# Kernel tuning notes

Hardware: AMD Instinct MI355X
Metric: run time of the kernel (lower is better)

Reference implementation:

```python
import jax, jax.numpy as jnp
import numpy as np

NUM_CLASSES = 80
BATCH_PER_IMG = 512          # cfg.MODEL.ROI_HEADS.BATCH_SIZE_PER_IMAGE
POS_FRAC = 0.25              # cfg.MODEL.ROI_HEADS.POSITIVE_FRACTION
NUM_FG_TARGET = int(BATCH_PER_IMG * POS_FRAC)  # 128
IOU_THRESH = 0.5             # cfg.MODEL.ROI_HEADS.IOU_THRESHOLDS = [0.5], labels [0,1]

B, M, N = 64, 100, 4000      # images, gt boxes/img, proposals/img
K = N + M                    # proposal_append_gt=True


def _make_boxes(key, shape, lo=0.0, hi=800.0, wh_max=256.0):
    k1, k2 = jax.random.split(key)
    xy = jax.random.uniform(k1, shape, minval=lo, maxval=hi)
    wh = jax.random.uniform(k2, shape, minval=8.0, maxval=wh_max)
    return jnp.concatenate([xy, xy + wh], axis=-1)  # [..., 4] = x1,y1,x2,y2


def setup_inputs() -> dict:
    key = jax.random.key(0)
    kg, kp, kc, kr = jax.random.split(key, 4)
    gt_boxes = _make_boxes(kg, (B, M, 2))
    proposal_boxes = _make_boxes(kp, (B, N, 2))
    gt_classes = jax.random.randint(kc, (B, M), 0, NUM_CLASSES, dtype=jnp.int32).astype(jnp.int64)
    rand_priority = jax.random.uniform(kr, (B, K), dtype=jnp.float32)
    return {
        'gt_boxes': gt_boxes,
        'proposal_boxes': proposal_boxes,
        'gt_classes': gt_classes,
        'rand_priority': rand_priority,
    }


def pairwise_iou(a, b):
    # a: [M,4], b: [K,4] -> [M,K]
    area_a = (a[:, 2] - a[:, 0]) * (a[:, 3] - a[:, 1])          # [M]
    area_b = (b[:, 2] - b[:, 0]) * (b[:, 3] - b[:, 1])          # [K]
    lt = jnp.maximum(a[:, None, :2], b[None, :, :2])            # [M,K,2]
    rb = jnp.minimum(a[:, None, 2:], b[None, :, 2:])            # [M,K,2]
    wh = jnp.clip(rb - lt, 0.0)
    inter = wh[..., 0] * wh[..., 1]                              # [M,K]
    union = area_a[:, None] + area_b[None, :] - inter
    return jnp.where(inter > 0, inter / union, 0.0)


def _per_image(gt_b, prop_b, gt_cls, pri):
    # proposal_append_gt: concat gt boxes onto proposals
    boxes = jnp.concatenate([prop_b, gt_b], axis=0)              # [K,4]
    quality = pairwise_iou(gt_b, boxes)                          # [M,K]
    matched_vals = quality.max(axis=0)                           # [K]
    matched_idxs = quality.argmax(axis=0)                        # [K]
    matched_labels = matched_vals >= IOU_THRESH                  # label 1 = fg, 0 = bg
    # gt_classes[matched_idxs]; bg gets label num_classes
    cls = jnp.where(matched_labels, gt_cls[matched_idxs], NUM_CLASSES)  # [K]
    fg = matched_labels
    bg = ~matched_labels
    num_fg = jnp.minimum(NUM_FG_TARGET, fg.sum())
    num_bg = jnp.minimum(BATCH_PER_IMG - num_fg, bg.sum())
    # randperm-equivalent: sort a shared random priority, masked per group
    fg_order = jnp.argsort(jnp.where(fg, pri, -1.0))[::-1]       # fg indices first
    bg_order = jnp.argsort(jnp.where(bg, pri, -1.0))[::-1]
    pos = jnp.arange(BATCH_PER_IMG)
    idx = jnp.where(pos < num_fg, fg_order[pos],
                    bg_order[jnp.clip(pos - num_fg, 0, K - 1)])
    valid = pos < (num_fg + num_bg)
    s_iou = jnp.where(valid, matched_vals[idx], 0.0)
    s_idx = jnp.where(valid, idx, -1)
    s_cls = jnp.where(valid, cls[idx], -1)
    s_gt = jnp.where(valid, matched_idxs[idx], -1)
    return s_iou, s_idx, s_cls, s_gt, valid


def reference(gt_boxes, proposal_boxes, gt_classes, rand_priority):
    return jax.vmap(_per_image)(gt_boxes, proposal_boxes,
                                gt_classes.astype(jnp.int32), rand_priority)
```

## Files before the change

### kernel.cpp

```cpp
#include <hip/hip_runtime.h>
#include <stdint.h>

#define B_IMG        64
#define M_GT         100
#define N_PROP       4000
#define K_TOT        4100
#define NUM_CLASSES_ 80
#define BATCH_PER    512
#define NUM_FG_TGT   128
#define OUT_STRIDE   (B_IMG * BATCH_PER)

#define NT1          256
#define BPI1         33
#define EPB1         128
#define NTH          1024
#define HALF_CAP     1024
#define KITER        ((K_TOT + NTH - 1) / NTH)
#define NTF          1024


__device__ __forceinline__ float iou_a(float4 g, float area_a,
                                       float bx1, float by1, float bx2, float by2,
                                       float area_b) {
#pragma clang fp contract(off)
    float ltx = fmaxf(g.x, bx1), lty = fmaxf(g.y, by1);
    float rbx = fminf(g.z, bx2), rby = fminf(g.w, by2);
    float wx = fmaxf(rbx - ltx, 0.0f);
    float wy = fmaxf(rby - lty, 0.0f);
    float inter = wx * wy;
    float uni = area_a + area_b - inter;
    return inter / uni;
}

__device__ __forceinline__ float iou_g(float4 g,
                                       float bx1, float by1, float bx2, float by2,
                                       float area_b) {
#pragma clang fp contract(off)
    float area_a = (g.z - g.x) * (g.w - g.y);
    float ltx = fmaxf(g.x, bx1), lty = fmaxf(g.y, by1);
    float rbx = fminf(g.z, bx2), rby = fminf(g.w, by2);
    float wx = fmaxf(rbx - ltx, 0.0f);
    float wy = fmaxf(rby - lty, 0.0f);
    float inter = wx * wy;
    float uni = area_a + area_b - inter;
    return inter / uni;
}

__device__ __forceinline__ float box_area(float4 g) {
#pragma clang fp contract(off)
    return (g.z - g.x) * (g.w - g.y);
}

__global__ __launch_bounds__(NT1, 8) void match_kernel(
        const float* __restrict__ gt_boxes,
        const float* __restrict__ prop_boxes,
        const float* __restrict__ rand_pri,
        uint64_t*    __restrict__ keys)
{
    __shared__ float4 s_gtb4[M_GT];
    __shared__ float  s_gta[M_GT];

    const int blk = blockIdx.x;
    const int b   = blk / BPI1;
    const int q   = blk % BPI1;
    const int tid = threadIdx.x;

    for (int i = tid; i < M_GT; i += NT1)
        s_gtb4[i] = ((const float4*)gt_boxes)[(size_t)b * M_GT + i];
    __syncthreads();
    for (int i = tid; i < M_GT; i += NT1)
        s_gta[i] = box_area(s_gtb4[i]);
    __syncthreads();

    const int e    = q * EPB1 + (tid >> 1);
    const int half = tid & 1;
    if (e >= K_TOT) return;

    const uint32_t pb = __float_as_uint(rand_pri[(size_t)b * K_TOT + e]);
    float4 bp;
    if (e < N_PROP)
        bp = *(const float4*)(prop_boxes + ((size_t)b * N_PROP + e) * 4);
    else
        bp = s_gtb4[e - N_PROP];
    const float area_b = box_area(bp);
    const int mlo = half * (M_GT / 2);
    float best = -1.0f; int bidx = mlo;
#pragma unroll 2
    for (int m = mlo; m < mlo + M_GT / 2; ++m) {
        float iv = iou_a(s_gtb4[m], s_gta[m], bp.x, bp.y, bp.z, bp.w, area_b);
        if (iv > best) { best = iv; bidx = m; }
    }
    const float ob = __shfl_xor(best, 1);
    const int   oi = __shfl_xor(bidx, 1);
    if (half == 0) {
        if (ob > best) { best = ob; bidx = oi; }
        const bool fg = best >= 0.5f;
        uint64_t key = (fg ? (1ull << 50) : 0ull)
                     | ((uint64_t)pb << 20)
                     | ((uint64_t)e  << 7)
                     | (uint64_t)bidx;
        __hip_atomic_store(&keys[(size_t)b * K_TOT + e], key,
                           __ATOMIC_RELAXED, __HIP_MEMORY_SCOPE_AGENT);
    }
}

__global__ __launch_bounds__(NTH) void select_kernel(
        const float* __restrict__ gt_boxes,
        const float* __restrict__ prop_boxes,
        const int*   __restrict__ gt_classes,
        const uint64_t* __restrict__ keys,
        float*       __restrict__ out)
{
    __shared__ uint64_t s_keys[K_TOT];
    __shared__ uint64_t s_cand[2 * HALF_CAP];
    __shared__ int      s_hist[2][256];
    __shared__ float4   s_gtb4[M_GT];
    __shared__ float    s_gta[M_GT];
    __shared__ int      s_gtc[M_GT];
    __shared__ float    s_out[5][BATCH_PER];
    __shared__ int      s_T[2], s_needed[2], s_cnt[2];

    const int b   = blockIdx.x;
    const int tid = threadIdx.x;

    __builtin_amdgcn_fence(__ATOMIC_ACQUIRE, "agent");

    for (int i = tid; i < 512; i += NTH) s_hist[i >> 8][i & 255] = 0;
    if (tid < 2) s_cnt[tid] = 0;
    for (int i = tid; i < M_GT; i += NTH) {
        s_gtb4[i] = ((const float4*)gt_boxes)[(size_t)b * M_GT + i];
        s_gtc[i]  = gt_classes[(size_t)b * M_GT + i];
    }
    __syncthreads();
    for (int i = tid; i < M_GT; i += NTH)
        s_gta[i] = box_area(s_gtb4[i]);

#pragma unroll
    for (int kb = 0; kb < KITER; ++kb) {
        int k = kb * NTH + tid;
        if (k < K_TOT) {
            uint64_t key = keys[(size_t)b * K_TOT + k];
            s_keys[k] = key;
            int g = ((key >> 50) & 1ull) ? 0 : 1;
            uint32_t pbits = (uint32_t)((key >> 20) & 0x3FFFFFFFull);
            int bucket = min(255, (int)(__uint_as_float(pbits) * 256.0f));
            atomicAdd(&s_hist[g][bucket], 1);
        }
    }
    __syncthreads();

    for (int d = 1; d < 256; d <<= 1) {
        int v = 0, g = tid >> 8, t = tid & 255;
        bool act = (tid < 512) && (t + d < 256);
        if (act) v = s_hist[g][t + d];
        __syncthreads();
        if (act) s_hist[g][t] += v;
        __syncthreads();
    }

    if (tid == 0) {
        int fg_total = s_hist[0][0];
        int bg_total = s_hist[1][0];
        int nfg = min(NUM_FG_TGT, fg_total);
        int nbg = min(BATCH_PER - nfg, bg_total);
        s_needed[0] = nfg; s_needed[1] = nbg;
    }
    __syncthreads();

    if (tid < 512) {
        int g = tid >> 8, t = tid & 255;
        int need = s_needed[g];
        int St  = s_hist[g][t];
        int St1 = (t == 255) ? -1 : s_hist[g][t + 1];
        if (St >= need && St1 < need) s_T[g] = t;
    }
    if (tid < BATCH_PER) {
        s_out[0][tid] = 0.0f; s_out[1][tid] = -1.0f;
        s_out[2][tid] = -1.0f; s_out[3][tid] = -1.0f;
    }
    __syncthreads();

    const int nfg = s_needed[0], nbg = s_needed[1];
    if (tid < BATCH_PER)
        s_out[4][tid] = (tid < nfg + nbg) ? 1.0f : 0.0f;

    const int lane = tid & 63;
    const uint64_t ltm = (1ull << lane) - 1ull;
#pragma unroll
    for (int kb = 0; kb < KITER; ++kb) {
        int k = kb * NTH + tid;
        bool in = k < K_TOT;
        uint64_t key = in ? s_keys[k] : 0ull;
        bool isfg = in && (((key >> 50) & 1ull) != 0ull);
        bool sel = false;
        if (in) {
            uint32_t pbits = (uint32_t)((key >> 20) & 0x3FFFFFFFull);
            int bucket = min(255, (int)(__uint_as_float(pbits) * 256.0f));
            sel = bucket >= s_T[isfg ? 0 : 1];
        }
        const bool sf = sel && isfg;
        const bool sb = sel && !isfg;
        const uint64_t bf = __ballot(sf);
        const uint64_t bb = __ballot(sb);
        int basef = 0, baseb = 0;
        if (lane == 0) {
            if (bf) basef = atomicAdd(&s_cnt[0], (int)__popcll(bf));
            if (bb) baseb = atomicAdd(&s_cnt[1], (int)__popcll(bb));
        }
        basef = __shfl(basef, 0);
        baseb = __shfl(baseb, 0);
        if (sf) {
            int pos = basef + (int)__popcll(bf & ltm);
            if (pos < HALF_CAP) s_cand[pos] = key;
        }
        if (sb) {
            int pos = baseb + (int)__popcll(bb & ltm);
            if (pos < HALF_CAP) s_cand[HALF_CAP + pos] = key;
        }
    }
    __syncthreads();

    const int fgc = min(s_cnt[0], HALF_CAP);
    const int bgc = min(s_cnt[1], HALF_CAP);
    for (int c = tid; c < fgc + bgc; c += NTH) {
        const bool isfg = (c < fgc);
        const int  base = isfg ? 0 : HALF_CAP;
        const int  cnt  = isfg ? fgc : bgc;
        const int  ci   = isfg ? c : (c - fgc);
        const uint64_t kc = s_cand[base + ci];
        int r = 0;
        for (int j = 0; j < cnt; ++j)
            r += (s_cand[base + j] > kc) ? 1 : 0;
        int slot = -1;
        if (isfg) { if (r < nfg) slot = r; }
        else      { if (r < nbg) slot = nfg + r; }
        if (slot >= 0) {
            int idx = (int)((kc >> 7) & 0x1FFFull);
            int mi  = (int)(kc & 0x7Full);
            float4 bp;
            if (idx < N_PROP)
                bp = *(const float4*)(prop_boxes + ((size_t)b * N_PROP + idx) * 4);
            else
                bp = s_gtb4[idx - N_PROP];
            const float area_b = box_area(bp);
            float iou = iou_a(s_gtb4[mi], s_gta[mi], bp.x, bp.y, bp.z, bp.w, area_b);
            s_out[0][slot] = iou;
            s_out[1][slot] = (float)idx;
            s_out[2][slot] = (float)(isfg ? s_gtc[mi] : NUM_CLASSES_);
            s_out[3][slot] = (float)mi;
        }
    }
    __syncthreads();

    for (int i = tid; i < 5 * BATCH_PER; i += NTH) {
        int o = i / BATCH_PER, p = i % BATCH_PER;
        out[(size_t)o * OUT_STRIDE + (size_t)b * BATCH_PER + p] = s_out[o][p];
    }
}

__global__ __launch_bounds__(NTF) void roiheads_fallback(
        const float* __restrict__ gt_boxes,
        const float* __restrict__ prop_boxes,
        const int*   __restrict__ gt_classes,
        const float* __restrict__ rand_pri,
        float*       __restrict__ out)
{
    __shared__ uint64_t s_keys[K_TOT];
    __shared__ uint64_t s_cand[2 * HALF_CAP];
    __shared__ int      s_hist[2][256];
    __shared__ float4   s_gtb4[M_GT];
    __shared__ int      s_gtc[M_GT];
    __shared__ float    s_out[5][BATCH_PER];
    __shared__ int      s_T[2], s_needed[2], s_cnt[2];

    const int b   = blockIdx.x;
    const int tid = threadIdx.x;

    for (int i = tid; i < 512; i += NTF) s_hist[i >> 8][i & 255] = 0;
    if (tid < 2) s_cnt[tid] = 0;
    for (int i = tid; i < M_GT; i += NTF) {
        s_gtb4[i] = ((const float4*)gt_boxes)[(size_t)b * M_GT + i];
        s_gtc[i]  = gt_classes[(size_t)b * M_GT + i];
    }
    __syncthreads();

    for (int k = tid; k < K_TOT; k += NTF) {
        float4 bp;
        if (k < N_PROP)
            bp = *(const float4*)(prop_boxes + ((size_t)b * N_PROP + k) * 4);
        else
            bp = s_gtb4[k - N_PROP];
        const float area_b = box_area(bp);
        float best = -1.0f; int bidx = 0;
        for (int m = 0; m < M_GT; ++m) {
            float iv = iou_g(s_gtb4[m], bp.x, bp.y, bp.z, bp.w, area_b);
            if (iv > best) { best = iv; bidx = m; }
        }
        const bool fg = best >= 0.5f;
        const float pri = rand_pri[(size_t)b * K_TOT + k];
        const uint32_t pb = __float_as_uint(pri);
        s_keys[k] = (fg ? (1ull << 50) : 0ull)
                  | ((uint64_t)pb << 20)
                  | ((uint64_t)k  << 7)
                  | (uint64_t)bidx;
        int bucket = min(255, (int)(pri * 256.0f));
        atomicAdd(&s_hist[fg ? 0 : 1][bucket], 1);
    }
    __syncthreads();

    for (int d = 1; d < 256; d <<= 1) {
        int v = 0, g = tid >> 8, t = tid & 255;
        bool act = (tid < 512) && (t + d < 256);
        if (act) v = s_hist[g][t + d];
        __syncthreads();
        if (act) s_hist[g][t] += v;
        __syncthreads();
    }

    if (tid == 0) {
        int fg_total = s_hist[0][0];
        int bg_total = s_hist[1][0];
        int nfg = min(NUM_FG_TGT, fg_total);
        int nbg = min(BATCH_PER - nfg, bg_total);
        s_needed[0] = nfg; s_needed[1] = nbg;
    }
    __syncthreads();

    if (tid < 512) {
        int g = tid >> 8, t = tid & 255;
        int need = s_needed[g];
        int St  = s_hist[g][t];
        int St1 = (t == 255) ? -1 : s_hist[g][t + 1];
        if (St >= need && St1 < need) s_T[g] = t;
    }
    if (tid < BATCH_PER) {
        s_out[0][tid] = 0.0f; s_out[1][tid] = -1.0f;
        s_out[2][tid] = -1.0f; s_out[3][tid] = -1.0f;
    }
    __syncthreads();

    const int nfg = s_needed[0], nbg = s_needed[1];
    if (tid < BATCH_PER)
        s_out[4][tid] = (tid < nfg + nbg) ? 1.0f : 0.0f;

    for (int k = tid; k < K_TOT; k += NTF) {
        uint64_t key = s_keys[k];
        int g = ((key >> 50) & 1ull) ? 0 : 1;
        uint32_t pbits = (uint32_t)((key >> 20) & 0x3FFFFFFFull);
        int bucket = min(255, (int)(__uint_as_float(pbits) * 256.0f));
        if (bucket >= s_T[g]) {
            int pos = atomicAdd(&s_cnt[g], 1);
            if (pos < HALF_CAP) s_cand[g * HALF_CAP + pos] = key;
        }
    }
    __syncthreads();

    const int fgc = min(s_cnt[0], HALF_CAP);
    const int bgc = min(s_cnt[1], HALF_CAP);
    for (int c = tid; c < fgc + bgc; c += NTF) {
        const bool isfg = (c < fgc);
        const int  base = isfg ? 0 : HALF_CAP;
        const int  cnt  = isfg ? fgc : bgc;
        const int  ci   = isfg ? c : (c - fgc);
        const uint64_t kc = s_cand[base + ci];
        int r = 0;
        for (int j = 0; j < cnt; ++j)
            r += (s_cand[base + j] > kc) ? 1 : 0;
        int slot = -1;
        if (isfg) { if (r < nfg) slot = r; }
        else      { if (r < nbg) slot = nfg + r; }
        if (slot >= 0) {
            int idx = (int)((kc >> 7) & 0x1FFFull);
            int mi  = (int)(kc & 0x7Full);
            float4 bp;
            if (idx < N_PROP)
                bp = *(const float4*)(prop_boxes + ((size_t)b * N_PROP + idx) * 4);
            else
                bp = s_gtb4[idx - N_PROP];
            const float area_b = box_area(bp);
            float iou = iou_g(s_gtb4[mi], bp.x, bp.y, bp.z, bp.w, area_b);
            s_out[0][slot] = iou;
            s_out[1][slot] = (float)idx;
            s_out[2][slot] = (float)(isfg ? s_gtc[mi] : NUM_CLASSES_);
            s_out[3][slot] = (float)mi;
        }
    }
    __syncthreads();

    for (int i = tid; i < 5 * BATCH_PER; i += NTF) {
        int o = i / BATCH_PER, p = i % BATCH_PER;
        out[(size_t)o * OUT_STRIDE + (size_t)b * BATCH_PER + p] = s_out[o][p];
    }
}

extern "C" void kernel_launch(void* const* d_in, const int* in_sizes, int n_in,
                              void* d_out, int out_size, void* d_ws, size_t ws_size,
                              hipStream_t stream) {
    const float* gt_boxes   = (const float*)d_in[0];
    const float* prop_boxes = (const float*)d_in[1];
    const int*   gt_classes = (const int*)  d_in[2];
    const float* rand_pri   = (const float*)d_in[3];
    float* out = (float*)d_out;

    const size_t need_ws = (size_t)B_IMG * K_TOT * sizeof(uint64_t);
    if (d_ws != nullptr && ws_size >= need_ws) {
        uint64_t* keys = (uint64_t*)d_ws;
        match_kernel<<<B_IMG * BPI1, NT1, 0, stream>>>(gt_boxes, prop_boxes,
                                                       rand_pri, keys);
        select_kernel<<<B_IMG, NTH, 0, stream>>>(gt_boxes, prop_boxes,
                                                 gt_classes, keys, out);
    } else {
        roiheads_fallback<<<B_IMG, NTF, 0, stream>>>(gt_boxes, prop_boxes,
                                                     gt_classes, rand_pri, out);
    }
}
```

Baseline: 105.2 us.

## Use one thread per proposal in matching and simplify candidate compaction

The matching kernel now gives each proposal a single thread that loops over all 100 GT boxes, reading them from global memory rather than shared memory, instead of splitting the GT range across two lanes and merging with shuffles. The grid per image drops from 33 to 17 blocks. The select kernel's ballot/popcount wave-aggregated compaction is replaced by plain per-thread shared atomics. This removes the shuffle and merge overhead and some synchronisation, but halves thread-level parallelism in matching and adds contention on the shared atomics.

```diff
diff --git a/kernel.cpp b/kernel.cpp
--- a/kernel.cpp
+++ b/kernel.cpp
@@ -11,8 +11,7 @@
 #define OUT_STRIDE   (B_IMG * BATCH_PER)
 
 #define NT1          256
-#define BPI1         33
-#define EPB1         128
+#define BPI1         17
 #define NTH          1024
 #define HALF_CAP     1024
 #define KITER        ((K_TOT + NTH - 1) / NTH)
@@ -57,23 +56,20 @@
         const float* __restrict__ rand_pri,
         uint64_t*    __restrict__ keys)
 {
-    __shared__ float4 s_gtb4[M_GT];
-    __shared__ float  s_gta[M_GT];
+    __shared__ float s_gta[M_GT];
 
     const int blk = blockIdx.x;
     const int b   = blk / BPI1;
     const int q   = blk % BPI1;
     const int tid = threadIdx.x;
 
+    const float4* gtb = (const float4*)gt_boxes + (size_t)b * M_GT;
+
     for (int i = tid; i < M_GT; i += NT1)
-        s_gtb4[i] = ((const float4*)gt_boxes)[(size_t)b * M_GT + i];
-    __syncthreads();
-    for (int i = tid; i < M_GT; i += NT1)
-        s_gta[i] = box_area(s_gtb4[i]);
-    __syncthreads();
-
-    const int e    = q * EPB1 + (tid >> 1);
-    const int half = tid & 1;
+        s_gta[i] = box_area(gtb[i]);
+    __syncthreads();
+
+    const int e = q * NT1 + tid;
     if (e >= K_TOT) return;
 
     const uint32_t pb = __float_as_uint(rand_pri[(size_t)b * K_TOT + e]);
@@ -81,27 +77,23 @@
     if (e < N_PROP)
         bp = *(const float4*)(prop_boxes + ((size_t)b * N_PROP + e) * 4);
     else
-        bp = s_gtb4[e - N_PROP];
+        bp = gtb[e - N_PROP];
     const float area_b = box_area(bp);
-    const int mlo = half * (M_GT / 2);
-    float best = -1.0f; int bidx = mlo;
-#pragma unroll 2
-    for (int m = mlo; m < mlo + M_GT / 2; ++m) {
-        float iv = iou_a(s_gtb4[m], s_gta[m], bp.x, bp.y, bp.z, bp.w, area_b);
+
+    float best = -1.0f; int bidx = 0;
+#pragma unroll 4
+    for (int m = 0; m < M_GT; ++m) {
+        const float4 g = gtb[m];
+        float iv = iou_a(g, s_gta[m], bp.x, bp.y, bp.z, bp.w, area_b);
         if (iv > best) { best = iv; bidx = m; }
     }
-    const float ob = __shfl_xor(best, 1);
-    const int   oi = __shfl_xor(bidx, 1);
-    if (half == 0) {
-        if (ob > best) { best = ob; bidx = oi; }
-        const bool fg = best >= 0.5f;
-        uint64_t key = (fg ? (1ull << 50) : 0ull)
-                     | ((uint64_t)pb << 20)
-                     | ((uint64_t)e  << 7)
-                     | (uint64_t)bidx;
-        __hip_atomic_store(&keys[(size_t)b * K_TOT + e], key,
-                           __ATOMIC_RELAXED, __HIP_MEMORY_SCOPE_AGENT);
-    }
+    const bool fg = best >= 0.5f;
+    uint64_t key = (fg ? (1ull << 50) : 0ull)
+                 | ((uint64_t)pb << 20)
+                 | ((uint64_t)e  << 7)
+                 | (uint64_t)bidx;
+    __hip_atomic_store(&keys[(size_t)b * K_TOT + e], key,
+                       __ATOMIC_RELAXED, __HIP_MEMORY_SCOPE_AGENT);
 }
 
 __global__ __launch_bounds__(NTH) void select_kernel(
@@ -184,38 +176,14 @@
     if (tid < BATCH_PER)
         s_out[4][tid] = (tid < nfg + nbg) ? 1.0f : 0.0f;
 
-    const int lane = tid & 63;
-    const uint64_t ltm = (1ull << lane) - 1ull;
-#pragma unroll
-    for (int kb = 0; kb < KITER; ++kb) {
-        int k = kb * NTH + tid;
-        bool in = k < K_TOT;
-        uint64_t key = in ? s_keys[k] : 0ull;
-        bool isfg = in && (((key >> 50) & 1ull) != 0ull);
-        bool sel = false;
-        if (in) {
-            uint32_t pbits = (uint32_t)((key >> 20) & 0x3FFFFFFFull);
-            int bucket = min(255, (int)(__uint_as_float(pbits) * 256.0f));
-            sel = bucket >= s_T[isfg ? 0 : 1];
-        }
-        const bool sf = sel && isfg;
-        const bool sb = sel && !isfg;
-        const uint64_t bf = __ballot(sf);
-        const uint64_t bb = __ballot(sb);
-        int basef = 0, baseb = 0;
-        if (lane == 0) {
-            if (bf) basef = atomicAdd(&s_cnt[0], (int)__popcll(bf));
-            if (bb) baseb = atomicAdd(&s_cnt[1], (int)__popcll(bb));
-        }
-        basef = __shfl(basef, 0);
-        baseb = __shfl(baseb, 0);
-        if (sf) {
-            int pos = basef + (int)__popcll(bf & ltm);
-            if (pos < HALF_CAP) s_cand[pos] = key;
-        }
-        if (sb) {
-            int pos = baseb + (int)__popcll(bb & ltm);
-            if (pos < HALF_CAP) s_cand[HALF_CAP + pos] = key;
+    for (int k = tid; k < K_TOT; k += NTH) {
+        uint64_t key = s_keys[k];
+        int g = ((key >> 50) & 1ull) ? 0 : 1;
+        uint32_t pbits = (uint32_t)((key >> 20) & 0x3FFFFFFFull);
+        int bucket = min(255, (int)(__uint_as_float(pbits) * 256.0f));
+        if (bucket >= s_T[g]) {
+            int pos = atomicAdd(&s_cnt[g], 1);
+            if (pos < HALF_CAP) s_cand[g * HALF_CAP + pos] = key;
         }
     }
     __syncthreads();
```

Measured after the change: 105.9 us. No clear change (+0.7%).
